# Kernel optimization log

Measured on AMD Instinct MI355X. Metric: run time of the kernel, lower is better.

The kernel has to match this reference:

```python
import jax, jax.numpy as jnp
import numpy as np

B, IN, H, K = 4096, 1024, 1024, 32  # batch, input_size, hidden_size, inner_hidden


def setup_inputs() -> dict:
    key = jax.random.key(0)
    ks = jax.random.split(key, 11)
    stdv = 1.0 / np.sqrt(H)
    u = lambda k, shp: jax.random.uniform(k, shp, jnp.float32, -stdv, stdv)
    return {
        "x": jax.random.normal(ks[0], (B, IN), jnp.float32),
        "h_prev": jax.random.normal(ks[1], (B, H), jnp.float32),
        "c_prev": jax.random.normal(ks[2], (B, H), jnp.float32),
        "Wg": u(ks[3], (3 * H, IN + H)),
        "bg": u(ks[4], (3 * H,)),
        "Wc": u(ks[5], (2 * H, IN + H)),
        "bc": u(ks[6], (2 * H,)),
        "W1": u(ks[7], (K, 2)),
        "b1": u(ks[8], (K,)),
        "W2": u(ks[9], (1, K)),
        "b2": u(ks[10], (1,)),
    }


def reference(x, h_prev, c_prev, Wg, bg, Wc, bc, W1, b1, W2, b2):
    combined = jnp.concatenate([x, h_prev], axis=1)          # [B, IN+H]
    gates = combined @ Wg.T + bg                              # [B, 3H]
    i, f, o = jnp.split(jax.nn.sigmoid(gates), 3, axis=1)     # each [B, H]
    cell_raw = combined @ Wc.T + bc                           # [B, 2H]
    pairs = cell_raw.reshape(B, H, 2)                         # [B, H, 2]
    hid = jax.nn.relu(jnp.einsum('bhp,kp->bhk', pairs, W1) + b1)  # [B, H, K]
    g = jnp.einsum('bhk,ok->bho', hid, W2)[..., 0] + b2[0]    # [B, H]
    c_next = f * c_prev + i * g
    h_next = o * jnp.tanh(c_next)
    return (h_next, c_next)
```

## Files before the change

### kernel.cpp

```cpp
#include <hip/hip_runtime.h>
#include <hip/hip_bf16.h>

#define BB   4096
#define INW  1024
#define HH   1024
#define KIN  2048
#define NG   5120
#define KH   32
#define FPG  10
#define NTG  32

typedef __bf16 bf16;
typedef __bf16 bf16x4 __attribute__((ext_vector_type(4)));
typedef __bf16 bf16x8 __attribute__((ext_vector_type(8)));
typedef float  floatx4 __attribute__((ext_vector_type(4)));

#define GLD16(gp, lp)                                                          \
  __builtin_amdgcn_global_load_lds(                                            \
      (__attribute__((address_space(1))) const void*)(gp),                     \
      (__attribute__((address_space(3))) void*)(lp), 16, 0, 0)

#define NCB  4096
#define NWB  1280

__global__ __launch_bounds__(256) void prep(
    const float* __restrict__ x, const float* __restrict__ h,
    const float* __restrict__ Wg, const float* __restrict__ Wc,
    bf16* __restrict__ comb, bf16* __restrict__ Wb) {
  int tid = threadIdx.x;
  if (blockIdx.x < NCB) {
    int e = (blockIdx.x * 256 + tid) * 8;
    int b = e >> 11;
    int c = e & (KIN - 1);
    const float* src = (c < INW) ? (x + (size_t)b * INW + c)
                                 : (h + (size_t)b * HH + (c - INW));
    float4 v0 = *(const float4*)src;
    float4 v1 = *(const float4*)(src + 4);
    bf16x8 ov;
    ov[0] = (bf16)v0.x; ov[1] = (bf16)v0.y; ov[2] = (bf16)v0.z; ov[3] = (bf16)v0.w;
    ov[4] = (bf16)v1.x; ov[5] = (bf16)v1.y; ov[6] = (bf16)v1.z; ov[7] = (bf16)v1.w;
    *(bf16x8*)(comb + e) = ov;
  } else {
    int w   = blockIdx.x - NCB;
    int nt  = w / 40;
    int rem = w - nt * 40;
    int f   = rem >> 2;
    int rp  = rem & 3;
    int q   = f / 5;
    int g   = f - q * 5;
    int kk  = tid >> 2;
    int kq  = tid & 3;
    size_t wbase = ((size_t)(nt * FPG + f) * 64 + kk) * 64 + kq * 16;
#pragma unroll
    for (int r4 = 0; r4 < 4; ++r4) {
      int s    = rp * 4 + r4;
      int hcol = nt * 32 + q * 16 + s;
      const float* src = (g < 3)
          ? (Wg + (size_t)(g * HH + hcol) * KIN + tid * 8)
          : (Wc + (size_t)(2 * hcol + (g - 3)) * KIN + tid * 8);
      float4 v0 = *(const float4*)src;
      float4 v1 = *(const float4*)(src + 4);
      bf16x8 ov;
      ov[0] = (bf16)v0.x; ov[1] = (bf16)v0.y; ov[2] = (bf16)v0.z; ov[3] = (bf16)v0.w;
      ov[4] = (bf16)v1.x; ov[5] = (bf16)v1.y; ov[6] = (bf16)v1.z; ov[7] = (bf16)v1.w;
      *(bf16x8*)(Wb + (wbase + s) * 8) = ov;
    }
  }
}

#define ASZ  8192

__global__ __launch_bounds__(256, 2) void gemm_fused(
    const bf16* __restrict__ A, const bf16* __restrict__ Bm,
    const float* __restrict__ c_prev, const float* __restrict__ bg,
    const float* __restrict__ bc, const float* __restrict__ W1,
    const float* __restrict__ b1, const float* __restrict__ W2,
    const float* __restrict__ b2, float* __restrict__ h_next,
    float* __restrict__ c_next) {
  __shared__ bf16 As2[2 * ASZ];

  const int tid  = threadIdx.x;
  const int wave = tid >> 6;
  const int lane = tid & 63;

  const int bid = blockIdx.y * gridDim.x + blockIdx.x;
  const int swz = (bid & 7) * 128 + (bid >> 3);
  const int m0  = (swz & 31) * 128;
  const int nt  = swz >> 5;

  const int wm = (wave >> 1) * 64;
  const int q  = wave & 1;
  const int lr = lane & 15;
  const int qd = lane >> 4;

  const bf16* Bq = Bm + (size_t)(nt * FPG + q * 5) * 32768 + (size_t)lane * 8;

  floatx4 acc[4][5] = {};
  bf16x8 bA[2][5], bB[2][5];

  const int arow0 = tid >> 3;
  const int acol  = tid & 7;

#define LOADB(buf, kt)                                                         \
  {                                                                            \
    _Pragma("unroll")                                                          \
    for (int ks = 0; ks < 2; ++ks)                                             \
      _Pragma("unroll")                                                        \
      for (int ni = 0; ni < 5; ++ni)                                           \
        buf[ks][ni] = *(const bf16x8*)(Bq + (size_t)ni * 32768 +               \
                                       (size_t)((kt) * 2 + ks) * 512);         \
  }

#define STAGEA(bb, kt)                                                         \
  {                                                                            \
    _Pragma("unroll")                                                          \
    for (int j = 0; j < 4; ++j) {                                              \
      int row = arow0 + j * 32;                                                \
      int c   = acol ^ (row & 7);                                              \
      GLD16(A + (size_t)(m0 + row) * KIN + (kt) * 64 + c * 8,                  \
            As2 + (size_t)(bb) * ASZ + (size_t)(j * 256 + wave * 64) * 8);     \
    }                                                                          \
  }

#define COMPUTE(bb, buf)                                                       \
  {                                                                            \
    const bf16* As = As2 + (size_t)(bb) * ASZ;                                 \
    _Pragma("unroll")                                                          \
    for (int ks = 0; ks < 2; ++ks) {                                           \
      bf16x8 af[4];                                                            \
      _Pragma("unroll")                                                        \
      for (int mi = 0; mi < 4; ++mi) {                                         \
        int row  = wm + mi * 16 + lr;                                          \
        int slot = (ks * 4 + qd) ^ (lr & 7);                                   \
        af[mi] = *(const bf16x8*)&As[(row << 6) + (slot << 3)];                \
      }                                                                        \
      _Pragma("unroll")                                                        \
      for (int mi = 0; mi < 4; ++mi)                                           \
        _Pragma("unroll")                                                      \
        for (int ni = 0; ni < 5; ++ni)                                         \
          acc[mi][ni] = __builtin_amdgcn_mfma_f32_16x16x32_bf16(               \
              af[mi], buf[ks][ni], acc[mi][ni], 0, 0, 0);                      \
    }                                                                          \
  }

  LOADB(bA, 0);
  STAGEA(0, 0);
  __syncthreads();

  for (int kt2 = 0; kt2 < 15; ++kt2) {
    LOADB(bB, 2 * kt2 + 1);
    STAGEA(1, 2 * kt2 + 1);
    COMPUTE(0, bA);
    __syncthreads();
    LOADB(bA, 2 * kt2 + 2);
    STAGEA(0, 2 * kt2 + 2);
    COMPUTE(1, bB);
    __syncthreads();
  }
  LOADB(bB, 31);
  STAGEA(1, 31);
  COMPUTE(0, bA);
  __syncthreads();
  COMPUTE(1, bB);

  const int h   = nt * 32 + q * 16 + lr;
  const float bgi = bg[h];
  const float bgf = bg[HH + h];
  const float bgo = bg[2 * HH + h];
  const float bc0 = bc[2 * h];
  const float bc1 = bc[2 * h + 1];
  const float gb  = b2[0];

  float p0[16], p1[16], ga[16];
#pragma unroll
  for (int mi = 0; mi < 4; ++mi)
#pragma unroll
    for (int r = 0; r < 4; ++r) {
      p0[mi * 4 + r] = acc[mi][3][r] + bc0;
      p1[mi * 4 + r] = acc[mi][4][r] + bc1;
      ga[mi * 4 + r] = gb;
    }
#pragma unroll
  for (int k = 0; k < KH; ++k) {
    float w0 = W1[2 * k], w1 = W1[2 * k + 1], bk = b1[k], wk = W2[k];
#pragma unroll
    for (int e = 0; e < 16; ++e) {
      float hv = fmaf(p0[e], w0, fmaf(p1[e], w1, bk));
      hv = fmaxf(hv, 0.0f);
      ga[e] = fmaf(hv, wk, ga[e]);
    }
  }

#pragma unroll
  for (int mi = 0; mi < 4; ++mi)
#pragma unroll
    for (int r = 0; r < 4; ++r) {
      int b    = m0 + wm + mi * 16 + qd * 4 + r;
      size_t o = (size_t)b * HH + h;
      float si = 1.0f / (1.0f + __expf(-(acc[mi][0][r] + bgi)));
      float sf = 1.0f / (1.0f + __expf(-(acc[mi][1][r] + bgf)));
      float so = 1.0f / (1.0f + __expf(-(acc[mi][2][r] + bgo)));
      float cn = fmaf(sf, c_prev[o], si * ga[mi * 4 + r]);
      float e2 = __expf(2.0f * cn);
      float th = 1.0f - 2.0f / (e2 + 1.0f);
      h_next[o] = so * th;
      c_next[o] = cn;
    }
}

extern "C" void kernel_launch(void* const* d_in, const int* in_sizes, int n_in,
                              void* d_out, int out_size, void* d_ws, size_t ws_size,
                              hipStream_t stream) {
  const float* x      = (const float*)d_in[0];
  const float* h_prev = (const float*)d_in[1];
  const float* c_prev = (const float*)d_in[2];
  const float* Wg     = (const float*)d_in[3];
  const float* bg     = (const float*)d_in[4];
  const float* Wc     = (const float*)d_in[5];
  const float* bc     = (const float*)d_in[6];
  const float* W1     = (const float*)d_in[7];
  const float* b1     = (const float*)d_in[8];
  const float* W2     = (const float*)d_in[9];
  const float* b2     = (const float*)d_in[10];
  float* out = (float*)d_out;

  char* ws = (char*)d_ws;
  bf16* comb = (bf16*)ws;
  bf16* Wb   = (bf16*)(ws + (size_t)BB * KIN * 2);

  prep<<<NCB + NWB, 256, 0, stream>>>(x, h_prev, Wg, Wc, comb, Wb);

  dim3 grid(BB / 128, NTG);
  gemm_fused<<<grid, 256, 0, stream>>>(comb, Wb, c_prev, bg, bc, W1, b1, W2,
                                       b2, out, out + (size_t)BB * HH);
}
```

Before: 250.4 us.

## Deepen A-tile LDS pipeline to four buffers with manual vmcnt waits

Grows the shared-memory A staging area from two to four buffers so A tiles are prefetched two k-steps ahead via global_load_lds. The two __syncthreads per pair of steps become one barrier per step with an explicit partial vmcnt wait, so loads stay in flight while MFMAs run. The loop is unrolled by four with register B buffers ping-ponging. The cost is doubled LDS use (64KB per block), which may cut occupancy below the two blocks per CU requested by the launch bounds. The hand-counted vmcnt and the redundant clamped loads at the tail also risk correctness if the count is off.

Measured after the change: 257.2 us. 2.7% more time.

```diff
diff --git a/kernel.cpp b/kernel.cpp
--- a/kernel.cpp
+++ b/kernel.cpp
@@ -77,7 +77,7 @@
     const float* __restrict__ b1, const float* __restrict__ W2,
     const float* __restrict__ b2, float* __restrict__ h_next,
     float* __restrict__ c_next) {
-  __shared__ bf16 As2[2 * ASZ];
+  __shared__ bf16 As2[4 * ASZ];
 
   const int tid  = threadIdx.x;
   const int wave = tid >> 6;
@@ -96,7 +96,7 @@
   const bf16* Bq = Bm + (size_t)(nt * FPG + q * 5) * 32768 + (size_t)lane * 8;
 
   floatx4 acc[4][5] = {};
-  bf16x8 bA[2][5], bB[2][5];
+  bf16x8 bregA[2][5], bregB[2][5];
 
   const int arow0 = tid >> 3;
   const int acol  = tid & 7;
@@ -143,25 +143,35 @@
     }                                                                          \
   }
 
-  LOADB(bA, 0);
+#define ITER(u, bnext, bcur, t)                                                \
+  {                                                                            \
+    int tb = ((t) + 1 < 32) ? (t) + 1 : 31;          \
+    LOADB(bnext, tb);                                                          \
+    asm volatile("s_waitcnt vmcnt(14)" ::: "memory");                          \
+    __builtin_amdgcn_s_barrier();                                              \
+    __builtin_amdgcn_sched_barrier(0);                                         \
+    int ta = ((t) + 2 < 32) ? (t) + 2 : 31;          \
+    STAGEA(((u) + 2) & 3, ta);                                                 \
+    COMPUTE((u), bcur);                                                        \
+  }
+
   STAGEA(0, 0);
-  __syncthreads();
-
-  for (int kt2 = 0; kt2 < 15; ++kt2) {
-    LOADB(bB, 2 * kt2 + 1);
-    STAGEA(1, 2 * kt2 + 1);
-    COMPUTE(0, bA);
-    __syncthreads();
-    LOADB(bA, 2 * kt2 + 2);
-    STAGEA(0, 2 * kt2 + 2);
-    COMPUTE(1, bB);
-    __syncthreads();
-  }
-  LOADB(bB, 31);
-  STAGEA(1, 31);
-  COMPUTE(0, bA);
-  __syncthreads();
-  COMPUTE(1, bB);
+  STAGEA(1, 1);
+  LOADB(bregA, 0);
+  asm volatile("s_waitcnt vmcnt(0)" ::: "memory");
+  __builtin_amdgcn_s_barrier();
+  __builtin_amdgcn_sched_barrier(0);
+
+#pragma unroll 1
+  for (int trip = 0; trip < 8; ++trip) {
+    const int t0 = trip * 4;
+    ITER(0, bregB, bregA, t0 + 0);
+    ITER(1, bregA, bregB, t0 + 1);
+    ITER(2, bregB, bregA, t0 + 2);
+    ITER(3, bregA, bregB, t0 + 3);
+  }
+
+  asm volatile("s_waitcnt vmcnt(0)" ::: "memory");
 
   const int h   = nt * 32 + q * 16 + lr;
   const float bgi = bg[h];
```
